# Optimization experiments

Measured on AMD Instinct MI355X. Metric: run time of the kernel, lower is better.

## Reference

```python
import jax, jax.numpy as jnp
import numpy as np

# dims: B batch, R seq_num (MSA rows), L seq_len (residues), D emb_dim, C n_emb_2D, H heads
B, R, L, D, C, H = 1, 256, 384, 512, 256, 4
HD = D // H
SCALE = np.float32((HD ** -0.5) / np.sqrt(L))  # head-dim scaling * seqlen_scaling (1/sqrt(L))
EPS = 1e-5


def setup_inputs() -> dict:
    key = jax.random.key(0)
    ks = jax.random.split(key, 6)
    s = 0.02
    return {
        "x": jax.random.normal(ks[0], (B, R, L, D), jnp.float32),
        "pair_feat": jax.random.normal(ks[1], (B, L, L, C), jnp.float32),
        "attn_mask": jnp.ones((B, L), jnp.int32),
        "ln_msa_g": jnp.ones((D,), jnp.float32),
        "ln_msa_b": jnp.zeros((D,), jnp.float32),
        "ln_pair_g": jnp.ones((C,), jnp.float32),
        "ln_pair_b": jnp.zeros((C,), jnp.float32),
        "W_pair": jax.random.normal(ks[2], (C, H), jnp.float32) * s,  # stacked per-head [C,1] linears
        "W_v": jax.random.normal(ks[3], (D, D), jnp.float32) * s,     # stacked per-head [D,HD] value proj
        "W_out": jax.random.normal(ks[4], (D, D), jnp.float32) * s,   # to_out (bias=False)
    }


def _ln(x, g, b):
    mu = jnp.mean(x, axis=-1, keepdims=True)
    var = jnp.mean(jnp.square(x - mu), axis=-1, keepdims=True)
    return (x - mu) * jax.lax.rsqrt(var + EPS) * g + b


def reference(x, pair_feat, attn_mask, ln_msa_g, ln_msa_b, ln_pair_g, ln_pair_b, W_pair, W_v, W_out):
    # MHPair_to_MSA.forward (eval mode, dropout=0)
    msa = _ln(x, ln_msa_g, ln_msa_b)                                  # [B,R,L,D]
    pf = (pair_feat + jnp.swapaxes(pair_feat, 1, 2)) * 0.5            # symmetrize
    pf = _ln(pf, ln_pair_g, ln_pair_b)                                # [B,L,L,C]
    # pair-feature-derived attention logits (no QK^T)
    logits = jnp.einsum('bijc,ch->bhij', pf * SCALE, W_pair)          # [B,H,L,L]
    V = jnp.einsum('brld,de->brle', msa, W_v).reshape(B, R, L, H, HD) # [B,R,L,H,HD]
    mask2 = attn_mask[:, :, None] * attn_mask[:, None, :]             # [B,L,L]
    logits = jnp.where(mask2[:, None, :, :] == 0,
                       jnp.finfo(logits.dtype).min, logits)
    attn = jax.nn.softmax(logits, axis=-1)                            # [B,H,L,L]
    out = jnp.einsum('bhij,brjhd->brihd', attn, V).reshape(B, R, L, D)
    out = out @ W_out                                                 # to_out, bias=False
    return x + out                                                    # residual
```

## Files before the change

kernel.cpp:

```cpp
#include <hip/hip_runtime.h>

#define L_   384
#define D_   512
#define C_   256
#define H_   4
#define RR_  256
#define M1_  98304
#define LL2_ 147456
#define NPAIR_BLOCKS 18480

typedef __bf16 bf16x8 __attribute__((ext_vector_type(8)));
typedef float f32x4 __attribute__((ext_vector_type(4)));

__device__ __forceinline__ unsigned short f2bf_bits(float f) {
  union { float f; unsigned u; } v; v.f = f;
  return (unsigned short)((v.u + 0x7fffu + ((v.u >> 16) & 1u)) >> 16);
}
__device__ __forceinline__ __bf16 f2bf(float f) {
  union { unsigned short s; __bf16 b; } o; o.s = f2bf_bits(f);
  return o.b;
}

__device__ __forceinline__ float wave_sum(float v) {
#pragma unroll
  for (int o = 32; o > 0; o >>= 1) v += __shfl_xor(v, o);
  return v;
}
__device__ __forceinline__ float wave_max(float v) {
#pragma unroll
  for (int o = 32; o > 0; o >>= 1) v = fmaxf(v, __shfl_xor(v, o));
  return v;
}

__global__ __launch_bounds__(256) void ln_msa_kernel(
    const float* __restrict__ x, const float* __restrict__ g,
    const float* __restrict__ b, __bf16* __restrict__ msa) {
  int row = blockIdx.x * 4 + (threadIdx.x >> 6);
  int lane = threadIdx.x & 63;
  const float4* xr = (const float4*)(x + (size_t)row * D_ + lane * 8);
  float4 v0 = xr[0], v1 = xr[1];
  float s1 = v0.x + v0.y + v0.z + v0.w + v1.x + v1.y + v1.z + v1.w;
  float s2 = v0.x * v0.x + v0.y * v0.y + v0.z * v0.z + v0.w * v0.w +
             v1.x * v1.x + v1.y * v1.y + v1.z * v1.z + v1.w * v1.w;
#pragma unroll
  for (int o = 32; o > 0; o >>= 1) {
    s1 += __shfl_xor(s1, o);
    s2 += __shfl_xor(s2, o);
  }
  float mu = s1 * (1.0f / D_);
  float var = s2 * (1.0f / D_) - mu * mu;
  float rs = rsqrtf(var + 1e-5f);
  const float4* gp = (const float4*)(g + lane * 8);
  const float4* bp = (const float4*)(b + lane * 8);
  float4 g0 = gp[0], g1 = gp[1], b0 = bp[0], b1 = bp[1];
  float y[8];
  y[0] = (v0.x - mu) * rs * g0.x + b0.x;
  y[1] = (v0.y - mu) * rs * g0.y + b0.y;
  y[2] = (v0.z - mu) * rs * g0.z + b0.z;
  y[3] = (v0.w - mu) * rs * g0.w + b0.w;
  y[4] = (v1.x - mu) * rs * g1.x + b1.x;
  y[5] = (v1.y - mu) * rs * g1.y + b1.y;
  y[6] = (v1.z - mu) * rs * g1.z + b1.z;
  y[7] = (v1.w - mu) * rs * g1.w + b1.w;
  uint4 pk;
  pk.x = ((unsigned)f2bf_bits(y[1]) << 16) | f2bf_bits(y[0]);
  pk.y = ((unsigned)f2bf_bits(y[3]) << 16) | f2bf_bits(y[2]);
  pk.z = ((unsigned)f2bf_bits(y[5]) << 16) | f2bf_bits(y[4]);
  pk.w = ((unsigned)f2bf_bits(y[7]) << 16) | f2bf_bits(y[6]);
  *(uint4*)(msa + (size_t)row * D_ + lane * 8) = pk;
}

__global__ __launch_bounds__(256) void pair_logits_kernel(
    const float* __restrict__ pf, const int* __restrict__ mask,
    const float* __restrict__ g, const float* __restrict__ b,
    const float* __restrict__ Wp, float* __restrict__ logits) {
  unsigned wid = blockIdx.x * 4 + (threadIdx.x >> 6);
  int lane = threadIdx.x & 63;
  unsigned a = wid / 385u;
  unsigned c = wid - a * 385u;
  int i, j;
  if (c < 384u - a) { i = a; j = a + c; }
  else { i = 383 - a; j = i + (c - (384 - a)); }

  int c0 = lane * 4;
  float4 p1 = *(const float4*)(pf + ((size_t)i * L_ + j) * C_ + c0);
  float4 p2 = *(const float4*)(pf + ((size_t)j * L_ + i) * C_ + c0);
  float4 v;
  v.x = 0.5f * (p1.x + p2.x); v.y = 0.5f * (p1.y + p2.y);
  v.z = 0.5f * (p1.z + p2.z); v.w = 0.5f * (p1.w + p2.w);
  float s1 = v.x + v.y + v.z + v.w;
  float s2 = v.x * v.x + v.y * v.y + v.z * v.z + v.w * v.w;
#pragma unroll
  for (int o = 32; o > 0; o >>= 1) {
    s1 += __shfl_xor(s1, o);
    s2 += __shfl_xor(s2, o);
  }
  float mu = s1 * (1.0f / C_);
  float var = s2 * (1.0f / C_) - mu * mu;
  float rs = rsqrtf(var + 1e-5f);
  float4 gv = *(const float4*)(g + c0);
  float4 bv = *(const float4*)(b + c0);
  float y0 = (v.x - mu) * rs * gv.x + bv.x;
  float y1 = (v.y - mu) * rs * gv.y + bv.y;
  float y2 = (v.z - mu) * rs * gv.z + bv.z;
  float y3 = (v.w - mu) * rs * gv.w + bv.w;
  const float4* wp = (const float4*)Wp;
  float4 w0 = wp[c0], w1 = wp[c0 + 1], w2 = wp[c0 + 2], w3 = wp[c0 + 3];
  float4 t;
  t.x = y0 * w0.x + y1 * w1.x + y2 * w2.x + y3 * w3.x;
  t.y = y0 * w0.y + y1 * w1.y + y2 * w2.y + y3 * w3.y;
  t.z = y0 * w0.z + y1 * w1.z + y2 * w2.z + y3 * w3.z;
  t.w = y0 * w0.w + y1 * w1.w + y2 * w2.w + y3 * w3.w;
#pragma unroll
  for (int o = 32; o > 0; o >>= 1) {
    t.x += __shfl_xor(t.x, o);
    t.y += __shfl_xor(t.y, o);
    t.z += __shfl_xor(t.z, o);
    t.w += __shfl_xor(t.w, o);
  }
  if (lane < 8) {
    int h = lane & 3;
    int ii = (lane < 4) ? i : j;
    int jj = (lane < 4) ? j : i;
    bool ok = (mask[i] != 0) && (mask[j] != 0);
    const float NEG = -3.402823466e38f;
    const float SCALE = (float)(0.08838834764831845 / 19.595917942265423);
    float th = (h == 0) ? t.x : (h == 1) ? t.y : (h == 2) ? t.z : t.w;
    logits[(size_t)h * LL2_ + (size_t)ii * L_ + jj] = ok ? SCALE * th : NEG;
  }
}

__global__ __launch_bounds__(256) void softmax_kernel(
    const float* __restrict__ logits, __bf16* __restrict__ attn) {
  int wave = threadIdx.x >> 6, lane = threadIdx.x & 63;
  int row = blockIdx.x * 4 + wave;
  const float* lr = logits + (size_t)row * L_;
  float v[6];
#pragma unroll
  for (int t = 0; t < 6; ++t) v[t] = lr[lane + t * 64];
  float mx = v[0];
#pragma unroll
  for (int t = 1; t < 6; ++t) mx = fmaxf(mx, v[t]);
  mx = wave_max(mx);
  float s = 0.f;
#pragma unroll
  for (int t = 0; t < 6; ++t) { v[t] = __expf(v[t] - mx); s += v[t]; }
  s = wave_sum(s);
  float inv = 1.0f / s;
  __bf16* ar = attn + (size_t)row * L_;
#pragma unroll
  for (int t = 0; t < 6; ++t) ar[lane + t * 64] = f2bf(v[t] * inv);
}

__global__ __launch_bounds__(256) void wtrans_kernel(
    const float* __restrict__ Wv, const float* __restrict__ Wo,
    __bf16* __restrict__ WvT, __bf16* __restrict__ WoT) {
  int id = blockIdx.x * 256 + threadIdx.x;
  int m = id >> 18;
  int e = (id >> 9) & 511, d = id & 511;
  const float* W = m ? Wo : Wv;
  __bf16* T = m ? WoT : WvT;
  T[(size_t)e * 512 + d] = f2bf(W[(size_t)d * 512 + e]);
}

__device__ __forceinline__ void gload16(const void* g, void* l) {
  __builtin_amdgcn_global_load_lds(
      (const __attribute__((address_space(1))) void*)g,
      (__attribute__((address_space(3))) void*)l, 16, 0, 0);
}

template <int NT>
__device__ __forceinline__ void stage_part32(__bf16* s, const __bf16* g, size_t ld) {
  int tid = threadIdx.x;
#pragma unroll
  for (int i = 0; i < 2; ++i) {
    int cid = i * NT + tid;
    int row = cid >> 2, c = cid & 3;
    int cs = c ^ ((row >> 1) & 3);
    gload16(g + (size_t)row * ld + cs * 8, (char*)s + cid * 16);
  }
}

__device__ __forceinline__ bf16x8 frag_ld32(const __bf16* s, int row, int fk) {
  int c = (fk >> 3) ^ ((row >> 1) & 3);
  return *(const bf16x8*)((const char*)s + row * 64 + c * 16);
}


__device__ __forceinline__ void mainloop256(
    const __bf16* __restrict__ A, size_t ldA,
    const __bf16* __restrict__ B, size_t ldB,
    int K, __bf16* lds, f32x4 acc[8][4]) {
  int lane = threadIdx.x & 63, wave = threadIdx.x >> 6;
  int wm = (wave >> 2) * 128, wn = (wave & 3) * 64;
  int fr = lane & 15, fk = (lane >> 4) * 8;
  int nt = K >> 5;
  const int SLOT = 512 * 32;
#pragma unroll
  for (int t = 0; t < 3; ++t) {
    stage_part32<512>(lds + t * SLOT, A + t * 32, ldA);
    stage_part32<512>(lds + t * SLOT + 256 * 32, B + t * 32, ldB);
  }
  for (int t = 0; t < nt; ++t) {
    int rem = nt - 1 - t;
    if (rem >= 2)      asm volatile("s_waitcnt vmcnt(8)" ::: "memory");
    else if (rem == 1) asm volatile("s_waitcnt vmcnt(4)" ::: "memory");
    else               asm volatile("s_waitcnt vmcnt(0)" ::: "memory");
    __builtin_amdgcn_s_barrier();
    const __bf16* As = lds + (t & 3) * SLOT;
    const __bf16* Bs = As + 256 * 32;
    if (t + 3 < nt) {
      __bf16* d = lds + ((t + 3) & 3) * SLOT;
      stage_part32<512>(d, A + (size_t)(t + 3) * 32, ldA);
      stage_part32<512>(d + 256 * 32, B + (size_t)(t + 3) * 32, ldB);
    }
    bf16x8 bfv[4];
#pragma unroll
    for (int ni = 0; ni < 4; ++ni) bfv[ni] = frag_ld32(Bs, wn + ni * 16 + fr, fk);
#pragma unroll
    for (int half = 0; half < 2; ++half) {
      bf16x8 af[4];
#pragma unroll
      for (int mi = 0; mi < 4; ++mi)
        af[mi] = frag_ld32(As, wm + half * 64 + mi * 16 + fr, fk);
      __builtin_amdgcn_s_setprio(1);
#pragma unroll
      for (int mi = 0; mi < 4; ++mi)
#pragma unroll
        for (int ni = 0; ni < 4; ++ni)
          acc[half * 4 + mi][ni] = __builtin_amdgcn_mfma_f32_16x16x32_bf16(
              af[mi], bfv[ni], acc[half * 4 + mi][ni], 0, 0, 0);
      __builtin_amdgcn_s_setprio(0);
    }
  }
}

__device__ __forceinline__ void mainloop128(
    const __bf16* __restrict__ A, size_t ldA,
    const __bf16* __restrict__ B, size_t ldB,
    int K, __bf16* lds, f32x4 acc[4][4]) {
  int lane = threadIdx.x & 63, wave = threadIdx.x >> 6;
  int wm = (wave >> 1) * 64, wn = (wave & 1) * 64;
  int fr = lane & 15, fk = (lane >> 4) * 8;
  int nt = K >> 5;
  const int SLOT = 256 * 32;
#pragma unroll
  for (int t = 0; t < 3; ++t) {
    stage_part32<256>(lds + t * SLOT, A + t * 32, ldA);
    stage_part32<256>(lds + t * SLOT + 128 * 32, B + t * 32, ldB);
  }
  for (int t = 0; t < nt; ++t) {
    int rem = nt - 1 - t;
    if (rem >= 2)      asm volatile("s_waitcnt vmcnt(8)" ::: "memory");
    else if (rem == 1) asm volatile("s_waitcnt vmcnt(4)" ::: "memory");
    else               asm volatile("s_waitcnt vmcnt(0)" ::: "memory");
    __builtin_amdgcn_s_barrier();
    const __bf16* As = lds + (t & 3) * SLOT;
    const __bf16* Bs = As + 128 * 32;
    if (t + 3 < nt) {
      __bf16* d = lds + ((t + 3) & 3) * SLOT;
      stage_part32<256>(d, A + (size_t)(t + 3) * 32, ldA);
      stage_part32<256>(d + 128 * 32, B + (size_t)(t + 3) * 32, ldB);
    }
    bf16x8 bfv[4];
#pragma unroll
    for (int ni = 0; ni < 4; ++ni) bfv[ni] = frag_ld32(Bs, wn + ni * 16 + fr, fk);
#pragma unroll
    for (int half = 0; half < 2; ++half) {
      bf16x8 af[2];
#pragma unroll
      for (int mi = 0; mi < 2; ++mi)
        af[mi] = frag_ld32(As, wm + half * 32 + mi * 16 + fr, fk);
      __builtin_amdgcn_s_setprio(1);
#pragma unroll
      for (int mi = 0; mi < 2; ++mi)
#pragma unroll
        for (int ni = 0; ni < 4; ++ni)
          acc[half * 2 + mi][ni] = __builtin_amdgcn_mfma_f32_16x16x32_bf16(
              af[mi], bfv[ni], acc[half * 2 + mi][ni], 0, 0, 0);
      __builtin_amdgcn_s_setprio(0);
    }
  }
}

__device__ __forceinline__ unsigned xcd_swz_3072(unsigned bid) {
  return (bid & 7u) * 384u + (bid >> 3);
}
__device__ __forceinline__ unsigned xcd_swz_768(unsigned bid) {
  return (bid & 7u) * 96u + (bid >> 3);
}

__global__ __launch_bounds__(512, 1) void gemm_vt_kernel(
    const __bf16* __restrict__ WvT, const __bf16* __restrict__ msa,
    __bf16* __restrict__ VT) {
  __shared__ __bf16 lds[4 * 512 * 32];
  unsigned swz = xcd_swz_768(blockIdx.x + 2 * blockIdx.y);
  int m0 = (swz & 1) * 256;
  int n0 = (swz >> 1) * 256;
  f32x4 acc[8][4] = {};
  mainloop256(WvT + (size_t)m0 * D_, D_, msa + (size_t)n0 * D_, D_, D_, lds, acc);
  int lane = threadIdx.x & 63, wave = threadIdx.x >> 6;
  int wm = (wave >> 2) * 128, wn = (wave & 3) * 64;
  int cr = (lane >> 4) * 4, cc = lane & 15;
#pragma unroll
  for (int mi = 0; mi < 8; ++mi)
#pragma unroll
    for (int ni = 0; ni < 4; ++ni)
#pragma unroll
      for (int rr = 0; rr < 4; ++rr) {
        int row = m0 + wm + mi * 16 + cr + rr;
        int col = n0 + wn + ni * 16 + cc;
        VT[(size_t)row * M1_ + col] = f2bf(acc[mi][ni][rr]);
      }
}

__global__ __launch_bounds__(256) void attnv_kernel(
    const __bf16* __restrict__ attn, const __bf16* __restrict__ VT,
    __bf16* __restrict__ out2) {
  __shared__ __bf16 lds[4 * 256 * 32];
  unsigned swz = xcd_swz_3072(blockIdx.x + 3 * blockIdx.y);
  int it = swz % 3u;
  int rh = swz / 3u;
  int h = rh & 3, r = rh >> 2;
  const __bf16* A = attn + (size_t)h * LL2_ + (size_t)it * 128 * L_;
  const __bf16* Bt = VT + (size_t)(h * 128) * M1_ + (size_t)r * L_;
  f32x4 acc[4][4] = {};
  mainloop128(A, L_, Bt, M1_, L_, lds, acc);
  int lane = threadIdx.x & 63, wave = threadIdx.x >> 6;
  int wm = (wave >> 1) * 64, wn = (wave & 1) * 64;
  int cr = (lane >> 4) * 4, cc = lane & 15;
#pragma unroll
  for (int mi = 0; mi < 4; ++mi)
#pragma unroll
    for (int ni = 0; ni < 4; ++ni)
#pragma unroll
      for (int rr = 0; rr < 4; ++rr) {
        int row_i = it * 128 + wm + mi * 16 + cr + rr;
        int col = h * 128 + wn + ni * 16 + cc;
        out2[((size_t)r * L_ + row_i) * D_ + col] = f2bf(acc[mi][ni][rr]);
      }
}

__global__ __launch_bounds__(512, 1) void gemm_out_kernel(
    const __bf16* __restrict__ out2, const __bf16* __restrict__ WoT,
    const float* __restrict__ x, float* __restrict__ out) {
  __shared__ __bf16 lds[4 * 512 * 32];
  unsigned swz = xcd_swz_768(blockIdx.x + 2 * blockIdx.y);
  int n0 = (swz & 1) * 256;
  int m0 = (swz >> 1) * 256;
  f32x4 acc[8][4] = {};
  mainloop256(out2 + (size_t)m0 * D_, D_, WoT + (size_t)n0 * D_, D_, D_, lds, acc);
  int lane = threadIdx.x & 63, wave = threadIdx.x >> 6;
  int wm = (wave >> 2) * 128, wn = (wave & 3) * 64;
  int cr = (lane >> 4) * 4, cc = lane & 15;
#pragma unroll
  for (int mi = 0; mi < 8; ++mi)
#pragma unroll
    for (int ni = 0; ni < 4; ++ni)
#pragma unroll
      for (int rr = 0; rr < 4; ++rr) {
        int row = m0 + wm + mi * 16 + cr + rr;
        int col = n0 + wn + ni * 16 + cc;
        size_t idx = (size_t)row * D_ + col;
        out[idx] = x[idx] + acc[mi][ni][rr];
      }
}

extern "C" void kernel_launch(void* const* d_in, const int* in_sizes, int n_in,
                              void* d_out, int out_size, void* d_ws, size_t ws_size,
                              hipStream_t stream) {
  const float* x      = (const float*)d_in[0];
  const float* pair   = (const float*)d_in[1];
  const int*   mask   = (const int*)d_in[2];
  const float* g_msa  = (const float*)d_in[3];
  const float* b_msa  = (const float*)d_in[4];
  const float* g_pair = (const float*)d_in[5];
  const float* b_pair = (const float*)d_in[6];
  const float* Wp     = (const float*)d_in[7];
  const float* Wv     = (const float*)d_in[8];
  const float* Wo     = (const float*)d_in[9];
  float* out = (float*)d_out;

  char* p = (char*)d_ws;
  auto alloc = [&](size_t bytes) {
    char* r = p;
    p += (bytes + 255) & ~(size_t)255;
    return r;
  };
  __bf16* msa    = (__bf16*)alloc((size_t)M1_ * D_ * 2);
  __bf16* VT     = (__bf16*)alloc((size_t)D_ * M1_ * 2);
  float*  logits = (float*)alloc((size_t)H_ * LL2_ * 4);
  __bf16* attn   = (__bf16*)alloc((size_t)H_ * LL2_ * 2);
  __bf16* WvT    = (__bf16*)alloc((size_t)512 * 512 * 2);
  __bf16* WoT    = (__bf16*)alloc((size_t)512 * 512 * 2);
  __bf16* out2   = msa;

  wtrans_kernel<<<2048, 256, 0, stream>>>(Wv, Wo, WvT, WoT);
  ln_msa_kernel<<<M1_ / 4, 256, 0, stream>>>(x, g_msa, b_msa, msa);
  gemm_vt_kernel<<<dim3(2, M1_ / 256), 512, 0, stream>>>(WvT, msa, VT);
  pair_logits_kernel<<<NPAIR_BLOCKS, 256, 0, stream>>>(pair, mask, g_pair, b_pair, Wp, logits);
  softmax_kernel<<<(H_ * L_) / 4, 256, 0, stream>>>(logits, attn);
  attnv_kernel<<<dim3(3, RR_ * H_), 256, 0, stream>>>(attn, VT, out2);
  gemm_out_kernel<<<dim3(2, M1_ / 256), 512, 0, stream>>>(out2, WoT, x, out);
}
```

Measured before the change: 376.3 us.

## Fuse MSA layernorm into value-projection GEMM and drop msa intermediate

Removes the standalone LayerNorm kernel and its bf16 msa buffer by computing per-row mean/rstd inside the V projection GEMM and normalizing fp32 x on the fly into LDS as the B operand. The GEMM tile shrinks from 256x256/512 threads to 128x128/256 threads with a simple double buffer. This saves the msa write and re-read but makes each block re-read x (stats pass plus operand loads) once per output-column tile, relying on cache locality across blocks.

```diff
diff --git a/kernel.cpp b/kernel.cpp
--- a/kernel.cpp
+++ b/kernel.cpp
@@ -30,44 +30,6 @@
 #pragma unroll
   for (int o = 32; o > 0; o >>= 1) v = fmaxf(v, __shfl_xor(v, o));
   return v;
-}
-
-__global__ __launch_bounds__(256) void ln_msa_kernel(
-    const float* __restrict__ x, const float* __restrict__ g,
-    const float* __restrict__ b, __bf16* __restrict__ msa) {
-  int row = blockIdx.x * 4 + (threadIdx.x >> 6);
-  int lane = threadIdx.x & 63;
-  const float4* xr = (const float4*)(x + (size_t)row * D_ + lane * 8);
-  float4 v0 = xr[0], v1 = xr[1];
-  float s1 = v0.x + v0.y + v0.z + v0.w + v1.x + v1.y + v1.z + v1.w;
-  float s2 = v0.x * v0.x + v0.y * v0.y + v0.z * v0.z + v0.w * v0.w +
-             v1.x * v1.x + v1.y * v1.y + v1.z * v1.z + v1.w * v1.w;
-#pragma unroll
-  for (int o = 32; o > 0; o >>= 1) {
-    s1 += __shfl_xor(s1, o);
-    s2 += __shfl_xor(s2, o);
-  }
-  float mu = s1 * (1.0f / D_);
-  float var = s2 * (1.0f / D_) - mu * mu;
-  float rs = rsqrtf(var + 1e-5f);
-  const float4* gp = (const float4*)(g + lane * 8);
-  const float4* bp = (const float4*)(b + lane * 8);
-  float4 g0 = gp[0], g1 = gp[1], b0 = bp[0], b1 = bp[1];
-  float y[8];
-  y[0] = (v0.x - mu) * rs * g0.x + b0.x;
-  y[1] = (v0.y - mu) * rs * g0.y + b0.y;
-  y[2] = (v0.z - mu) * rs * g0.z + b0.z;
-  y[3] = (v0.w - mu) * rs * g0.w + b0.w;
-  y[4] = (v1.x - mu) * rs * g1.x + b1.x;
-  y[5] = (v1.y - mu) * rs * g1.y + b1.y;
-  y[6] = (v1.z - mu) * rs * g1.z + b1.z;
-  y[7] = (v1.w - mu) * rs * g1.w + b1.w;
-  uint4 pk;
-  pk.x = ((unsigned)f2bf_bits(y[1]) << 16) | f2bf_bits(y[0]);
-  pk.y = ((unsigned)f2bf_bits(y[3]) << 16) | f2bf_bits(y[2]);
-  pk.z = ((unsigned)f2bf_bits(y[5]) << 16) | f2bf_bits(y[4]);
-  pk.w = ((unsigned)f2bf_bits(y[7]) << 16) | f2bf_bits(y[6]);
-  *(uint4*)(msa + (size_t)row * D_ + lane * 8) = pk;
 }
 
 __global__ __launch_bounds__(256) void pair_logits_kernel(
@@ -169,6 +131,157 @@
       (__attribute__((address_space(3))) void*)l, 16, 0, 0);
 }
 
+__device__ __forceinline__ unsigned xcd_swz_3072(unsigned bid) {
+  return (bid & 7u) * 384u + (bid >> 3);
+}
+__device__ __forceinline__ unsigned xcd_swz_768(unsigned bid) {
+  return (bid & 7u) * 96u + (bid >> 3);
+}
+
+__global__ __launch_bounds__(256, 4) void gemm_vtln_kernel(
+    const __bf16* __restrict__ WvT, const float* __restrict__ x,
+    const float* __restrict__ g, const float* __restrict__ b,
+    __bf16* __restrict__ VT) {
+  __shared__ char lds[37888];
+  float* muS = (float*)(lds + 32768);
+  float* rsS = (float*)(lds + 33280);
+  float* gS  = (float*)(lds + 33792);
+  float* bS  = (float*)(lds + 35840);
+  unsigned swz = xcd_swz_3072(blockIdx.x + 4 * blockIdx.y);
+  int e0 = (swz & 3) * 128;
+  int m0 = (swz >> 2) * 128;
+  int tid = threadIdx.x, lane = tid & 63, wave = tid >> 6;
+
+  gS[tid] = g[tid]; gS[tid + 256] = g[tid + 256];
+  bS[tid] = b[tid]; bS[tid + 256] = b[tid + 256];
+
+  for (int ri = 0; ri < 32; ++ri) {
+    int row = wave * 32 + ri;
+    const float4* xr = (const float4*)(x + (size_t)(m0 + row) * D_ + lane * 8);
+    float4 a0 = xr[0], a1 = xr[1];
+    float s1 = a0.x + a0.y + a0.z + a0.w + a1.x + a1.y + a1.z + a1.w;
+    float s2 = a0.x * a0.x + a0.y * a0.y + a0.z * a0.z + a0.w * a0.w +
+               a1.x * a1.x + a1.y * a1.y + a1.z * a1.z + a1.w * a1.w;
+#pragma unroll
+    for (int o = 32; o > 0; o >>= 1) {
+      s1 += __shfl_xor(s1, o);
+      s2 += __shfl_xor(s2, o);
+    }
+    if (lane == 0) {
+      float mu = s1 * (1.0f / D_);
+      float var = s2 * (1.0f / D_) - mu * mu;
+      muS[row] = mu;
+      rsS[row] = rsqrtf(var + 1e-5f);
+    }
+  }
+  __syncthreads();
+
+  int row_u[2], kq_u[2];
+#pragma unroll
+  for (int u = 0; u < 2; ++u) {
+    int cid = u * 256 + tid;
+    row_u[u] = cid >> 2;
+    kq_u[u] = cid & 3;
+  }
+  float4 xr0[2], xr1[2];
+
+  auto issue_x = [&](int t) {
+#pragma unroll
+    for (int u = 0; u < 2; ++u) {
+      const float* src = x + (size_t)(m0 + row_u[u]) * D_ + t * 32 + kq_u[u] * 8;
+      xr0[u] = *(const float4*)(src);
+      xr1[u] = *(const float4*)(src + 4);
+    }
+  };
+  auto gloadA = [&](char* slot, int t) {
+#pragma unroll
+    for (int it = 0; it < 2; ++it) {
+      int cid = it * 256 + tid;
+      int row = cid >> 2, c = cid & 3;
+      gload16(WvT + (size_t)(e0 + row) * D_ + t * 32 + (c ^ (row & 3)) * 8,
+              slot + cid * 16);
+    }
+  };
+  auto ln_write = [&](char* slot, int t) {
+#pragma unroll
+    for (int u = 0; u < 2; ++u) {
+      int row = row_u[u], kq = kq_u[u];
+      float mu = muS[row], rs = rsS[row];
+      int kc = t * 32 + kq * 8;
+      float4 g0 = *(float4*)(gS + kc), g1 = *(float4*)(gS + kc + 4);
+      float4 b0 = *(float4*)(bS + kc), b1 = *(float4*)(bS + kc + 4);
+      float y[8];
+      y[0] = (xr0[u].x - mu) * rs * g0.x + b0.x;
+      y[1] = (xr0[u].y - mu) * rs * g0.y + b0.y;
+      y[2] = (xr0[u].z - mu) * rs * g0.z + b0.z;
+      y[3] = (xr0[u].w - mu) * rs * g0.w + b0.w;
+      y[4] = (xr1[u].x - mu) * rs * g1.x + b1.x;
+      y[5] = (xr1[u].y - mu) * rs * g1.y + b1.y;
+      y[6] = (xr1[u].z - mu) * rs * g1.z + b1.z;
+      y[7] = (xr1[u].w - mu) * rs * g1.w + b1.w;
+      uint4 pk;
+      pk.x = ((unsigned)f2bf_bits(y[1]) << 16) | f2bf_bits(y[0]);
+      pk.y = ((unsigned)f2bf_bits(y[3]) << 16) | f2bf_bits(y[2]);
+      pk.z = ((unsigned)f2bf_bits(y[5]) << 16) | f2bf_bits(y[4]);
+      pk.w = ((unsigned)f2bf_bits(y[7]) << 16) | f2bf_bits(y[6]);
+      *(uint4*)(slot + 8192 + row * 64 + ((kq ^ (row & 3)) * 16)) = pk;
+    }
+  };
+
+  f32x4 acc[4][4] = {};
+  int fr = lane & 15;
+  int ck = lane >> 4;
+  const int NT = D_ / 32;
+
+  issue_x(0);
+  gloadA(lds, 0);
+  asm volatile("s_waitcnt vmcnt(0)" ::: "memory");
+  ln_write(lds, 0);
+  __syncthreads();
+
+  for (int t = 0; t < NT; ++t) {
+    char* cur = lds + (t & 1) * 16384;
+    char* nxt = lds + ((t + 1) & 1) * 16384;
+    if (t + 1 < NT) {
+      issue_x(t + 1);
+      gloadA(nxt, t + 1);
+    }
+    bf16x8 af[4], bfv[4];
+#pragma unroll
+    for (int mi = 0; mi < 4; ++mi) {
+      int row = (wave >> 1) * 64 + mi * 16 + fr;
+      af[mi] = *(const bf16x8*)(cur + row * 64 + ((ck ^ (row & 3)) * 16));
+    }
+#pragma unroll
+    for (int ni = 0; ni < 4; ++ni) {
+      int row = (wave & 1) * 64 + ni * 16 + fr;
+      bfv[ni] = *(const bf16x8*)(cur + 8192 + row * 64 + ((ck ^ (row & 3)) * 16));
+    }
+#pragma unroll
+    for (int mi = 0; mi < 4; ++mi)
+#pragma unroll
+      for (int ni = 0; ni < 4; ++ni)
+        acc[mi][ni] = __builtin_amdgcn_mfma_f32_16x16x32_bf16(af[mi], bfv[ni], acc[mi][ni], 0, 0, 0);
+    if (t + 1 < NT) {
+      asm volatile("s_waitcnt vmcnt(0)" ::: "memory");
+      ln_write(nxt, t + 1);
+    }
+    __syncthreads();
+  }
+
+  int cr = (lane >> 4) * 4, cc = lane & 15;
+#pragma unroll
+  for (int mi = 0; mi < 4; ++mi)
+#pragma unroll
+    for (int ni = 0; ni < 4; ++ni)
+#pragma unroll
+      for (int rr = 0; rr < 4; ++rr) {
+        int erow = e0 + (wave >> 1) * 64 + mi * 16 + cr + rr;
+        int mcol = m0 + (wave & 1) * 64 + ni * 16 + cc;
+        VT[(size_t)erow * M1_ + mcol] = f2bf(acc[mi][ni][rr]);
+      }
+}
+
 template <int NT>
 __device__ __forceinline__ void stage_part32(__bf16* s, const __bf16* g, size_t ld) {
   int tid = threadIdx.x;
@@ -185,7 +298,6 @@
   int c = (fk >> 3) ^ ((row >> 1) & 3);
   return *(const bf16x8*)((const char*)s + row * 64 + c * 16);
 }
-
 
 __device__ __forceinline__ void mainloop256(
     const __bf16* __restrict__ A, size_t ldA,
@@ -281,37 +393,6 @@
       __builtin_amdgcn_s_setprio(0);
     }
   }
-}
-
-__device__ __forceinline__ unsigned xcd_swz_3072(unsigned bid) {
-  return (bid & 7u) * 384u + (bid >> 3);
-}
-__device__ __forceinline__ unsigned xcd_swz_768(unsigned bid) {
-  return (bid & 7u) * 96u + (bid >> 3);
-}
-
-__global__ __launch_bounds__(512, 1) void gemm_vt_kernel(
-    const __bf16* __restrict__ WvT, const __bf16* __restrict__ msa,
-    __bf16* __restrict__ VT) {
-  __shared__ __bf16 lds[4 * 512 * 32];
-  unsigned swz = xcd_swz_768(blockIdx.x + 2 * blockIdx.y);
-  int m0 = (swz & 1) * 256;
-  int n0 = (swz >> 1) * 256;
-  f32x4 acc[8][4] = {};
-  mainloop256(WvT + (size_t)m0 * D_, D_, msa + (size_t)n0 * D_, D_, D_, lds, acc);
-  int lane = threadIdx.x & 63, wave = threadIdx.x >> 6;
-  int wm = (wave >> 2) * 128, wn = (wave & 3) * 64;
-  int cr = (lane >> 4) * 4, cc = lane & 15;
-#pragma unroll
-  for (int mi = 0; mi < 8; ++mi)
-#pragma unroll
-    for (int ni = 0; ni < 4; ++ni)
-#pragma unroll
-      for (int rr = 0; rr < 4; ++rr) {
-        int row = m0 + wm + mi * 16 + cr + rr;
-        int col = n0 + wn + ni * 16 + cc;
-        VT[(size_t)row * M1_ + col] = f2bf(acc[mi][ni][rr]);
-      }
 }
 
 __global__ __launch_bounds__(256) void attnv_kernel(
@@ -387,17 +468,15 @@
     p += (bytes + 255) & ~(size_t)255;
     return r;
   };
-  __bf16* msa    = (__bf16*)alloc((size_t)M1_ * D_ * 2);
   __bf16* VT     = (__bf16*)alloc((size_t)D_ * M1_ * 2);
+  __bf16* out2   = (__bf16*)alloc((size_t)M1_ * D_ * 2);
   float*  logits = (float*)alloc((size_t)H_ * LL2_ * 4);
   __bf16* attn   = (__bf16*)alloc((size_t)H_ * LL2_ * 2);
   __bf16* WvT    = (__bf16*)alloc((size_t)512 * 512 * 2);
   __bf16* WoT    = (__bf16*)alloc((size_t)512 * 512 * 2);
-  __bf16* out2   = msa;
 
   wtrans_kernel<<<2048, 256, 0, stream>>>(Wv, Wo, WvT, WoT);
-  ln_msa_kernel<<<M1_ / 4, 256, 0, stream>>>(x, g_msa, b_msa, msa);
-  gemm_vt_kernel<<<dim3(2, M1_ / 256), 512, 0, stream>>>(WvT, msa, VT);
+  gemm_vtln_kernel<<<dim3(4, M1_ / 128), 256, 0, stream>>>(WvT, x, g_msa, b_msa, VT);
   pair_logits_kernel<<<NPAIR_BLOCKS, 256, 0, stream>>>(pair, mask, g_pair, b_pair, Wp, logits);
   softmax_kernel<<<(H_ * L_) / 4, 256, 0, stream>>>(logits, attn);
   attnv_kernel<<<dim3(3, RR_ * H_), 256, 0, stream>>>(attn, VT, out2);
```

After: 458.7 us. +21.9%, slower.

## Switch 256-tile GEMM mainloop to two-stage double buffering with smaller LDS

Applied to the files above, without the earlier changes.

Replaces the four-slot, three-tiles-ahead LDS prefetch pipeline in the 256x256 GEMM mainloop with a two-slot double buffer, halving each block's shared memory. It also drops the minimum-blocks hint from launch bounds on the V-projection and output-projection kernels, apparently to let more blocks share a CU. The trade is a shallower prefetch depth, which hides less global-load latency. The large accumulator footprint may prevent any occupancy gain. The next tile is issued into the buffer read in the previous iteration before the barrier, which risks a read-after-write race unless the loop body ends with a barrier. The softmax wave reductions are inlined, with no speed effect.

```diff
diff --git a/kernel.cpp b/kernel.cpp
--- a/kernel.cpp
+++ b/kernel.cpp
@@ -19,17 +19,6 @@
 __device__ __forceinline__ __bf16 f2bf(float f) {
   union { unsigned short s; __bf16 b; } o; o.s = f2bf_bits(f);
   return o.b;
-}
-
-__device__ __forceinline__ float wave_sum(float v) {
-#pragma unroll
-  for (int o = 32; o > 0; o >>= 1) v += __shfl_xor(v, o);
-  return v;
-}
-__device__ __forceinline__ float wave_max(float v) {
-#pragma unroll
-  for (int o = 32; o > 0; o >>= 1) v = fmaxf(v, __shfl_xor(v, o));
-  return v;
 }
 
 __global__ __launch_bounds__(256) void ln_msa_kernel(
@@ -141,11 +130,13 @@
   float mx = v[0];
 #pragma unroll
   for (int t = 1; t < 6; ++t) mx = fmaxf(mx, v[t]);
-  mx = wave_max(mx);
+#pragma unroll
+  for (int o = 32; o > 0; o >>= 1) mx = fmaxf(mx, __shfl_xor(mx, o));
   float s = 0.f;
 #pragma unroll
   for (int t = 0; t < 6; ++t) { v[t] = __expf(v[t] - mx); s += v[t]; }
-  s = wave_sum(s);
+#pragma unroll
+  for (int o = 32; o > 0; o >>= 1) s += __shfl_xor(s, o);
   float inv = 1.0f / s;
   __bf16* ar = attn + (size_t)row * L_;
 #pragma unroll
@@ -169,6 +160,13 @@
       (__attribute__((address_space(3))) void*)l, 16, 0, 0);
 }
 
+__device__ __forceinline__ unsigned xcd_swz_3072(unsigned bid) {
+  return (bid & 7u) * 384u + (bid >> 3);
+}
+__device__ __forceinline__ unsigned xcd_swz_768(unsigned bid) {
+  return (bid & 7u) * 96u + (bid >> 3);
+}
+
 template <int NT>
 __device__ __forceinline__ void stage_part32(__bf16* s, const __bf16* g, size_t ld) {
   int tid = threadIdx.x;
@@ -186,8 +184,7 @@
   return *(const bf16x8*)((const char*)s + row * 64 + c * 16);
 }
 
-
-__device__ __forceinline__ void mainloop256(
+__device__ __forceinline__ void mainloop256_2s(
     const __bf16* __restrict__ A, size_t ldA,
     const __bf16* __restrict__ B, size_t ldB,
     int K, __bf16* lds, f32x4 acc[8][4]) {
@@ -196,24 +193,20 @@
   int fr = lane & 15, fk = (lane >> 4) * 8;
   int nt = K >> 5;
   const int SLOT = 512 * 32;
-#pragma unroll
-  for (int t = 0; t < 3; ++t) {
-    stage_part32<512>(lds + t * SLOT, A + t * 32, ldA);
-    stage_part32<512>(lds + t * SLOT + 256 * 32, B + t * 32, ldB);
-  }
+  stage_part32<512>(lds, A, ldA);
+  stage_part32<512>(lds + 256 * 32, B, ldB);
   for (int t = 0; t < nt; ++t) {
-    int rem = nt - 1 - t;
-    if (rem >= 2)      asm volatile("s_waitcnt vmcnt(8)" ::: "memory");
-    else if (rem == 1) asm volatile("s_waitcnt vmcnt(4)" ::: "memory");
-    else               asm volatile("s_waitcnt vmcnt(0)" ::: "memory");
+    const __bf16* As = lds + (t & 1) * SLOT;
+    const __bf16* Bs = As + 256 * 32;
+    if (t + 1 < nt) {
+      __bf16* d = lds + ((t + 1) & 1) * SLOT;
+      stage_part32<512>(d, A + (size_t)(t + 1) * 32, ldA);
+      stage_part32<512>(d + 256 * 32, B + (size_t)(t + 1) * 32, ldB);
+      asm volatile("s_waitcnt vmcnt(4)" ::: "memory");
+    } else {
+      asm volatile("s_waitcnt vmcnt(0)" ::: "memory");
+    }
     __builtin_amdgcn_s_barrier();
-    const __bf16* As = lds + (t & 3) * SLOT;
-    const __bf16* Bs = As + 256 * 32;
-    if (t + 3 < nt) {
-      __bf16* d = lds + ((t + 3) & 3) * SLOT;
-      stage_part32<512>(d, A + (size_t)(t + 3) * 32, ldA);
-      stage_part32<512>(d + 256 * 32, B + (size_t)(t + 3) * 32, ldB);
-    }
     bf16x8 bfv[4];
 #pragma unroll
     for (int ni = 0; ni < 4; ++ni) bfv[ni] = frag_ld32(Bs, wn + ni * 16 + fr, fk);
@@ -283,22 +276,15 @@
   }
 }
 
-__device__ __forceinline__ unsigned xcd_swz_3072(unsigned bid) {
-  return (bid & 7u) * 384u + (bid >> 3);
-}
-__device__ __forceinline__ unsigned xcd_swz_768(unsigned bid) {
-  return (bid & 7u) * 96u + (bid >> 3);
-}
-
-__global__ __launch_bounds__(512, 1) void gemm_vt_kernel(
+__global__ __launch_bounds__(512) void gemm_vt_kernel(
     const __bf16* __restrict__ WvT, const __bf16* __restrict__ msa,
     __bf16* __restrict__ VT) {
-  __shared__ __bf16 lds[4 * 512 * 32];
+  __shared__ __bf16 lds[2 * 512 * 32];
   unsigned swz = xcd_swz_768(blockIdx.x + 2 * blockIdx.y);
   int m0 = (swz & 1) * 256;
   int n0 = (swz >> 1) * 256;
   f32x4 acc[8][4] = {};
-  mainloop256(WvT + (size_t)m0 * D_, D_, msa + (size_t)n0 * D_, D_, D_, lds, acc);
+  mainloop256_2s(WvT + (size_t)m0 * D_, D_, msa + (size_t)n0 * D_, D_, D_, lds, acc);
   int lane = threadIdx.x & 63, wave = threadIdx.x >> 6;
   int wm = (wave >> 2) * 128, wn = (wave & 3) * 64;
   int cr = (lane >> 4) * 4, cc = lane & 15;
@@ -341,15 +327,15 @@
       }
 }
 
-__global__ __launch_bounds__(512, 1) void gemm_out_kernel(
+__global__ __launch_bounds__(512) void gemm_out_kernel(
     const __bf16* __restrict__ out2, const __bf16* __restrict__ WoT,
     const float* __restrict__ x, float* __restrict__ out) {
-  __shared__ __bf16 lds[4 * 512 * 32];
+  __shared__ __bf16 lds[2 * 512 * 32];
   unsigned swz = xcd_swz_768(blockIdx.x + 2 * blockIdx.y);
   int n0 = (swz & 1) * 256;
   int m0 = (swz >> 1) * 256;
   f32x4 acc[8][4] = {};
-  mainloop256(out2 + (size_t)m0 * D_, D_, WoT + (size_t)n0 * D_, D_, D_, lds, acc);
+  mainloop256_2s(out2 + (size_t)m0 * D_, D_, WoT + (size_t)n0 * D_, D_, D_, lds, acc);
   int lane = threadIdx.x & 63, wave = threadIdx.x >> 6;
   int wm = (wave >> 2) * 128, wn = (wave & 3) * 64;
   int cr = (lane >> 4) * 4, cc = lane & 15;
```

Measured after the change: 375.9 us. About the same (-0.1%).
